# Kernel optimization log

Measured on AMD Instinct MI355X. Metric: run time of the kernel, lower is better.

The kernel has to match this reference:

```python
import jax, jax.numpy as jnp
import numpy as np

T, B, S, V, D = 64, 32, 400, 32000, 1536  # timesteps, batch, post len, vocab, dh+2*eh


def setup_inputs() -> dict:
    key = jax.random.key(0)
    k0, k1, k2, k3, k4 = jax.random.split(key, 5)
    return {
        "h": jax.random.normal(k0, (T, B, D), jnp.float32),
        "W": jax.random.normal(k1, (D, V), jnp.float32) * 0.02,
        "b": jnp.zeros((V,), jnp.float32),
        # attention weights over post positions (rows sum to 1, like the model's softmax attention)
        "att": jax.nn.softmax(jax.random.normal(k2, (T, B, S), jnp.float32), axis=-1),
        # generation probability in (0,1)
        "p_gen": jax.nn.sigmoid(jax.random.normal(k3, (T, B, 1), jnp.float32)),
        # post token ids, seq-first (S, B) as in the original data layout
        "post": jax.random.randint(k4, (S, B), 0, V),
    }


def reference(h, W, b, att, p_gen, post):
    # gen.w = wLinearLayer(gen.h): (T,B,D) @ (D,V) + (V,)
    w = jnp.einsum('tbd,dv->tbv', h, W) + b
    # sum_on_voc_index: scatter-add att[t,b,s] into voc_att[t,b,post[s,b]].
    # (The torch code builds a dense (B,V,S) zero buffer, scatter_'s the same
    # positions every timestep and sums over S -- identical to this scatter-add.)
    idx = post.T                                   # (B, S)
    b_idx = jnp.arange(B)[:, None]                 # (B, 1) -> broadcasts with idx
    voc_att = jnp.zeros((T, B, V), w.dtype).at[:, b_idx, idx].add(att)
    # pointer-generator mixture
    return p_gen * w + (1.0 - p_gen) * voc_att
```

## Files before the change

kernel.cpp:

```cpp
#include <hip/hip_runtime.h>
#include <hip/hip_bf16.h>
#include <stdint.h>

#define T_DIM 64
#define B_DIM 32
#define S_DIM 400
#define V_DIM 32000
#define D_DIM 1536
#define M_DIM (T_DIM * B_DIM)

typedef __attribute__((ext_vector_type(8))) short bf16x8;
typedef __attribute__((ext_vector_type(4))) float f32x4;

#define MEMFENCE asm volatile("" ::: "memory")
#define BARRIER() do { MEMFENCE; __builtin_amdgcn_s_barrier(); MEMFENCE; } while (0)


static __device__ __forceinline__ unsigned short f2bf(float x) {
    union { float f; uint32_t u; } v; v.f = x;
    uint32_t r = (v.u + 0x7FFFu + ((v.u >> 16) & 1u)) >> 16;
    return (unsigned short)r;
}

static __device__ __forceinline__ void gload_lds16(const void* g, void* l) {
    __builtin_amdgcn_global_load_lds(
        (const __attribute__((address_space(1))) uint32_t*)g,
        (__attribute__((address_space(3))) uint32_t*)l,
        16, 0, 0);
}


__global__ void convert_h(const float* __restrict__ h, unsigned short* __restrict__ hb) {
    const size_t n4 = (size_t)M_DIM * D_DIM / 4;
    for (size_t i = (size_t)blockIdx.x * blockDim.x + threadIdx.x; i < n4;
         i += (size_t)gridDim.x * blockDim.x) {
        const float4 v = ((const float4*)h)[i];
        ushort4 o;
        o.x = f2bf(v.x); o.y = f2bf(v.y); o.z = f2bf(v.z); o.w = f2bf(v.w);
        ((ushort4*)hb)[i] = o;
    }
}


__global__ __launch_bounds__(256)
void convT_W(const float* __restrict__ W, unsigned short* __restrict__ Wt) {
    __shared__ unsigned short lds[64 * 66];
    const int k0 = blockIdx.x * 64;
    const int v0 = blockIdx.y * 64;
    const int tid = threadIdx.x;
    const int rr = tid >> 4;
    const int cc = (tid & 15) * 4;

    #pragma unroll
    for (int p = 0; p < 4; ++p) {
        const int r = p * 16 + rr;
        const float4 v = *(const float4*)&W[(size_t)(k0 + r) * V_DIM + v0 + cc];
        unsigned short* q = &lds[r * 66 + cc];
        q[0] = f2bf(v.x); q[1] = f2bf(v.y); q[2] = f2bf(v.z); q[3] = f2bf(v.w);
    }
    __syncthreads();
    #pragma unroll
    for (int p = 0; p < 4; ++p) {
        const int n = p * 16 + rr;
        ushort4 o;
        o.x = lds[(cc + 0) * 66 + n];
        o.y = lds[(cc + 1) * 66 + n];
        o.z = lds[(cc + 2) * 66 + n];
        o.w = lds[(cc + 3) * 66 + n];
        *(ushort4*)&Wt[(size_t)(v0 + n) * D_DIM + k0 + cc] = o;
    }
}


#define GBM 256
#define GBN 256
#define GBK 32
#define GNKT (D_DIM / GBK)

__global__ __launch_bounds__(512, 2)
void gemm_mfma256(const unsigned short* __restrict__ A,
                  const unsigned short* __restrict__ Bt,
                  const float* __restrict__ bias,
                  const float* __restrict__ p_gen,
                  float* __restrict__ out) {
    __shared__ unsigned short ldsA[4][GBM * GBK];
    __shared__ unsigned short ldsB[4][GBN * GBK];

    const int bid = blockIdx.x;
    const int swz = (bid & 7) * 125 + (bid >> 3);
    const int m0 = (swz & 7) * GBM;
    const int n0 = (swz >> 3) * GBN;

    const int tid = threadIdx.x;
    const int lane = tid & 63;
    const int wid = tid >> 6;
    const int wr = wid >> 2;
    const int wc = wid & 3;
    const int rq = lane & 15;
    const int kq = (lane >> 4) * 8;

    const char* gA[2]; const char* gB[2]; int ldsOff[2];
    #pragma unroll
    for (int j = 0; j < 2; ++j) {
        const int o = tid * 16 + j * 8192;
        const int row = o >> 6;
        const int lc = (o & 63) ^ (((row >> 1) & 3) << 4);
        gA[j] = (const char*)A + (size_t)(m0 + row) * D_DIM * 2 + lc;
        gB[j] = (const char*)Bt + (size_t)(n0 + row) * D_DIM * 2 + lc;
        ldsOff[j] = o;
    }

    #define STAGE2(kt, j)                                                        \
        do {                                                                     \
            const int _b = (kt) & 3;                                             \
            gload_lds16(gA[j] + (size_t)(kt) * (GBK * 2),                        \
                        (char*)&ldsA[_b][0] + ldsOff[j]);                        \
            gload_lds16(gB[j] + (size_t)(kt) * (GBK * 2),                        \
                        (char*)&ldsB[_b][0] + ldsOff[j]);                        \
        } while (0)

    int aOff0[4], aOff1[4], bOff[4];
    #pragma unroll
    for (int i = 0; i < 4; ++i) {
        int r0 = wr * 128 + i * 16 + rq;
        int r1 = r0 + 64;
        aOff0[i] = r0 * 64 + ((kq * 2) ^ (((r0 >> 1) & 3) << 4));
        aOff1[i] = r1 * 64 + ((kq * 2) ^ (((r1 >> 1) & 3) << 4));
        int rb = wc * 64 + i * 16 + rq;
        bOff[i] = rb * 64 + ((kq * 2) ^ (((rb >> 1) & 3) << 4));
    }

    f32x4 acc[8][4] = {};

    #pragma unroll
    for (int t = 0; t < 3; ++t) { STAGE2(t, 0); STAGE2(t, 1); }
    asm volatile("s_waitcnt vmcnt(8)" ::: "memory");
    BARRIER();

    for (int kt = 0; kt < GNKT; ++kt) {
        const char* As = (const char*)&ldsA[kt & 3][0];
        const char* Bs = (const char*)&ldsB[kt & 3][0];
        bf16x8 a[4], b[4];

        #pragma unroll
        for (int i = 0; i < 4; ++i) a[i] = *(const bf16x8*)(As + aOff0[i]);
        #pragma unroll
        for (int j = 0; j < 4; ++j) b[j] = *(const bf16x8*)(Bs + bOff[j]);
        if (kt + 3 < GNKT) STAGE2(kt + 3, 0);
        BARRIER();
        __builtin_amdgcn_s_setprio(1);
        #pragma unroll
        for (int mi = 0; mi < 4; ++mi)
            #pragma unroll
            for (int nj = 0; nj < 4; ++nj)
                acc[mi][nj] = __builtin_amdgcn_mfma_f32_16x16x32_bf16(a[mi], b[nj], acc[mi][nj], 0, 0, 0);
        __builtin_amdgcn_s_setprio(0);
        BARRIER();

        #pragma unroll
        for (int i = 0; i < 4; ++i) a[i] = *(const bf16x8*)(As + aOff1[i]);
        if (kt + 3 < GNKT) STAGE2(kt + 3, 1);
        BARRIER();
        __builtin_amdgcn_s_setprio(1);
        #pragma unroll
        for (int mi = 0; mi < 4; ++mi)
            #pragma unroll
            for (int nj = 0; nj < 4; ++nj)
                acc[4 + mi][nj] = __builtin_amdgcn_mfma_f32_16x16x32_bf16(a[mi], b[nj], acc[4 + mi][nj], 0, 0, 0);
        __builtin_amdgcn_s_setprio(0);

        if (kt < GNKT - 3)       { asm volatile("s_waitcnt vmcnt(8)" ::: "memory"); }
        else if (kt == GNKT - 3) { asm volatile("s_waitcnt vmcnt(4)" ::: "memory"); }
        else if (kt == GNKT - 2) { asm volatile("s_waitcnt vmcnt(0)" ::: "memory"); }
        BARRIER();
    }

    const int rr4 = (lane >> 4) * 4;
    #pragma unroll
    for (int mi = 0; mi < 8; ++mi) {
        #pragma unroll
        for (int r = 0; r < 4; ++r) {
            const int m = m0 + wr * 128 + mi * 16 + rr4 + r;
            const float pgv = p_gen[m];
            #pragma unroll
            for (int nj = 0; nj < 4; ++nj) {
                const int n = n0 + wc * 64 + nj * 16 + rq;
                out[(size_t)m * V_DIM + n] = pgv * (acc[mi][nj][r] + bias[n]);
            }
        }
    }
    #undef STAGE2
}


__global__ void scatter_att(const float* __restrict__ att, const float* __restrict__ p_gen,
                            const int* __restrict__ post, float* __restrict__ out) {
    const int tb = blockIdx.x;
    const int b = tb & (B_DIM - 1);
    const float g = 1.0f - p_gen[tb];
    float* o = out + (size_t)tb * V_DIM;
    const float* a = att + (size_t)tb * S_DIM;
    for (int s = threadIdx.x; s < S_DIM; s += blockDim.x) {
        atomicAdd(&o[post[s * B_DIM + b]], g * a[s]);
    }
}


#define FB_MT 16
__global__ __launch_bounds__(256)
void gemm_naive(const float* __restrict__ h, const float* __restrict__ W,
                const float* __restrict__ bias, const float* __restrict__ pg,
                float* __restrict__ out) {
    const int mb = blockIdx.y;
    const int v = blockIdx.x * 256 + threadIdx.x;
    __shared__ float hs[FB_MT][128];
    float acc[FB_MT] = {};
    for (int k0 = 0; k0 < D_DIM; k0 += 128) {
        for (int i = threadIdx.x; i < FB_MT * 128; i += 256)
            hs[i >> 7][i & 127] = h[(size_t)(mb * FB_MT + (i >> 7)) * D_DIM + k0 + (i & 127)];
        __syncthreads();
        for (int kk = 0; kk < 128; ++kk) {
            const float wv = W[(size_t)(k0 + kk) * V_DIM + v];
            #pragma unroll
            for (int i = 0; i < FB_MT; ++i) acc[i] += hs[i][kk] * wv;
        }
        __syncthreads();
    }
    #pragma unroll
    for (int i = 0; i < FB_MT; ++i) {
        const int m = mb * FB_MT + i;
        out[(size_t)m * V_DIM + v] = pg[m] * (acc[i] + bias[v]);
    }
}


extern "C" void kernel_launch(void* const* d_in, const int* in_sizes, int n_in,
                              void* d_out, int out_size, void* d_ws, size_t ws_size,
                              hipStream_t stream) {
    const float* h    = (const float*)d_in[0];
    const float* W    = (const float*)d_in[1];
    const float* bias = (const float*)d_in[2];
    const float* att  = (const float*)d_in[3];
    const float* pg   = (const float*)d_in[4];
    const int*   post = (const int*)d_in[5];
    float* out = (float*)d_out;

    const size_t wt_bytes = (size_t)V_DIM * D_DIM * 2;
    const size_t hb_bytes = (size_t)M_DIM * D_DIM * 2;

    if (ws_size >= wt_bytes + hb_bytes) {
        unsigned short* Wt = (unsigned short*)d_ws;
        unsigned short* hb = (unsigned short*)((char*)d_ws + wt_bytes);
        convert_h<<<1024, 256, 0, stream>>>(h, hb);
        dim3 tg(D_DIM / 64, V_DIM / 64);
        convT_W<<<tg, 256, 0, stream>>>(W, Wt);
        gemm_mfma256<<<(M_DIM / GBM) * (V_DIM / GBN), 512, 0, stream>>>(hb, Wt, bias, pg, out);
    } else {
        dim3 fg(V_DIM / 256, M_DIM / FB_MT);
        gemm_naive<<<fg, 256, 0, stream>>>(h, W, bias, pg, out);
    }

    scatter_att<<<M_DIM, 256, 0, stream>>>(att, pg, post, out);
}
```

Measured before the change: 397.6 us.

## Software-pipeline LDS fragment reads across k-tiles and drop one barrier per step

Restructures the GEMM main loop so the next k-tile's A0/B fragments are read from LDS during the current tile's second MFMA phase, using double-buffered B registers (bE/bO) and a loop unrolled by two. The per-iteration barrier count falls from four to two, and the vmcnt waits are retuned to fit the new issue order. The aim is to hide LDS latency behind MFMA work and cut synchronisation stalls. In exchange it uses more registers, and the reordered waits and barriers add a risk of LDS buffer races.

```diff
diff --git a/kernel.cpp b/kernel.cpp
--- a/kernel.cpp
+++ b/kernel.cpp
@@ -130,62 +130,76 @@
         bOff[i] = rb * 64 + ((kq * 2) ^ (((rb >> 1) & 3) << 4));
     }
 
-    f32x4 acc[8][4] = {};
+    f32x4 accL[4][4] = {};
+    f32x4 accH[4][4] = {};
+    bf16x8 a0[4], a1[4], bE[4], bO[4];
+
+    auto read_a0b = [&](int kt, bf16x8 (&bb)[4]) {
+        const char* As_ = (const char*)&ldsA[kt & 3][0];
+        const char* Bs_ = (const char*)&ldsB[kt & 3][0];
+        #pragma unroll
+        for (int i = 0; i < 4; ++i) a0[i] = *(const bf16x8*)(As_ + aOff0[i]);
+        #pragma unroll
+        for (int i = 0; i < 4; ++i) bb[i] = *(const bf16x8*)(Bs_ + bOff[i]);
+    };
+    auto read_a1 = [&](int kt) {
+        const char* As_ = (const char*)&ldsA[kt & 3][0];
+        #pragma unroll
+        for (int i = 0; i < 4; ++i) a1[i] = *(const bf16x8*)(As_ + aOff1[i]);
+    };
+
+    auto tile_step = [&](int kt, bf16x8 (&bc)[4], bf16x8 (&bn)[4]) {
+        read_a1(kt);
+        if (kt + 3 < GNKT) STAGE2(kt + 3, 0);
+        BARRIER();
+        __builtin_amdgcn_s_setprio(1);
+        #pragma unroll
+        for (int mi = 0; mi < 4; ++mi)
+            #pragma unroll
+            for (int nj = 0; nj < 4; ++nj)
+                accL[mi][nj] = __builtin_amdgcn_mfma_f32_16x16x32_bf16(a0[mi], bc[nj], accL[mi][nj], 0, 0, 0);
+        __builtin_amdgcn_s_setprio(0);
+
+        if (kt < GNKT - 3)       { asm volatile("s_waitcnt vmcnt(6)" ::: "memory"); }
+        else if (kt == GNKT - 3) { asm volatile("s_waitcnt vmcnt(4)" ::: "memory"); }
+        else if (kt == GNKT - 2) { asm volatile("s_waitcnt vmcnt(0)" ::: "memory"); }
+        if (kt + 1 < GNKT) read_a0b(kt + 1, bn);
+        if (kt + 3 < GNKT) STAGE2(kt + 3, 1);
+        BARRIER();
+        __builtin_amdgcn_s_setprio(1);
+        #pragma unroll
+        for (int mi = 0; mi < 4; ++mi)
+            #pragma unroll
+            for (int nj = 0; nj < 4; ++nj)
+                accH[mi][nj] = __builtin_amdgcn_mfma_f32_16x16x32_bf16(a1[mi], bc[nj], accH[mi][nj], 0, 0, 0);
+        __builtin_amdgcn_s_setprio(0);
+    };
 
     #pragma unroll
     for (int t = 0; t < 3; ++t) { STAGE2(t, 0); STAGE2(t, 1); }
     asm volatile("s_waitcnt vmcnt(8)" ::: "memory");
     BARRIER();
-
-    for (int kt = 0; kt < GNKT; ++kt) {
-        const char* As = (const char*)&ldsA[kt & 3][0];
-        const char* Bs = (const char*)&ldsB[kt & 3][0];
-        bf16x8 a[4], b[4];
-
-        #pragma unroll
-        for (int i = 0; i < 4; ++i) a[i] = *(const bf16x8*)(As + aOff0[i]);
-        #pragma unroll
-        for (int j = 0; j < 4; ++j) b[j] = *(const bf16x8*)(Bs + bOff[j]);
-        if (kt + 3 < GNKT) STAGE2(kt + 3, 0);
-        BARRIER();
-        __builtin_amdgcn_s_setprio(1);
-        #pragma unroll
-        for (int mi = 0; mi < 4; ++mi)
-            #pragma unroll
-            for (int nj = 0; nj < 4; ++nj)
-                acc[mi][nj] = __builtin_amdgcn_mfma_f32_16x16x32_bf16(a[mi], b[nj], acc[mi][nj], 0, 0, 0);
-        __builtin_amdgcn_s_setprio(0);
-        BARRIER();
-
-        #pragma unroll
-        for (int i = 0; i < 4; ++i) a[i] = *(const bf16x8*)(As + aOff1[i]);
-        if (kt + 3 < GNKT) STAGE2(kt + 3, 1);
-        BARRIER();
-        __builtin_amdgcn_s_setprio(1);
-        #pragma unroll
-        for (int mi = 0; mi < 4; ++mi)
-            #pragma unroll
-            for (int nj = 0; nj < 4; ++nj)
-                acc[4 + mi][nj] = __builtin_amdgcn_mfma_f32_16x16x32_bf16(a[mi], b[nj], acc[4 + mi][nj], 0, 0, 0);
-        __builtin_amdgcn_s_setprio(0);
-
-        if (kt < GNKT - 3)       { asm volatile("s_waitcnt vmcnt(8)" ::: "memory"); }
-        else if (kt == GNKT - 3) { asm volatile("s_waitcnt vmcnt(4)" ::: "memory"); }
-        else if (kt == GNKT - 2) { asm volatile("s_waitcnt vmcnt(0)" ::: "memory"); }
-        BARRIER();
+    read_a0b(0, bE);
+
+    for (int kt = 0; kt < GNKT; kt += 2) {
+        tile_step(kt, bE, bO);
+        tile_step(kt + 1, bO, bE);
     }
 
     const int rr4 = (lane >> 4) * 4;
     #pragma unroll
-    for (int mi = 0; mi < 8; ++mi) {
+    for (int mi = 0; mi < 4; ++mi) {
         #pragma unroll
         for (int r = 0; r < 4; ++r) {
-            const int m = m0 + wr * 128 + mi * 16 + rr4 + r;
-            const float pgv = p_gen[m];
+            const int mL = m0 + wr * 128 + mi * 16 + rr4 + r;
+            const float pgL = p_gen[mL];
+            const int mH = mL + 64;
+            const float pgH = p_gen[mH];
             #pragma unroll
             for (int nj = 0; nj < 4; ++nj) {
                 const int n = n0 + wc * 64 + nj * 16 + rq;
-                out[(size_t)m * V_DIM + n] = pgv * (acc[mi][nj][r] + bias[n]);
+                out[(size_t)mL * V_DIM + n] = pgL * (accL[mi][nj][r] + bias[n]);
+                out[(size_t)mH * V_DIM + n] = pgH * (accH[mi][nj][r] + bias[n]);
             }
         }
     }
```

After: 387.2 us. -2.6%, faster.
